# Kernel optimization log

Hardware: AMD Instinct MI355X
Metric: run time of the kernel (lower is better)

Reference implementation:

```python
import jax, jax.numpy as jnp
import numpy as np

NODES, NFEAT = 128, 256


def setup_inputs() -> dict:
    key = jax.random.key(0)
    k1, k2, k3, k4, k5, k6 = jax.random.split(key, 6)
    B = 512
    x = jax.random.normal(k1, (B, NODES, NFEAT), dtype=jnp.float32)
    adj = jax.random.uniform(k2, (B, NODES, NODES), dtype=jnp.float32)
    # GraphConvolution(nfeat, nfeat): weight [nfeat, nfeat], bias [nfeat]
    s = 1.0 / np.sqrt(NFEAT)
    gcn_w = jax.random.uniform(k3, (NFEAT, NFEAT), minval=-s, maxval=s, dtype=jnp.float32)
    gcn_b = jax.random.uniform(k4, (NFEAT,), minval=-s, maxval=s, dtype=jnp.float32)
    # fc: Linear(nfeat*nodes, nfeat), torch layout [out, in]
    s2 = 1.0 / np.sqrt(NFEAT * NODES)
    fc_w = jax.random.uniform(k5, (NFEAT, NFEAT * NODES), minval=-s2, maxval=s2, dtype=jnp.float32)
    fc_b = jax.random.uniform(k6, (NFEAT,), minval=-s2, maxval=s2, dtype=jnp.float32)
    return {"x": x, "adj": adj, "gcn_w": gcn_w, "gcn_b": gcn_b, "fc_w": fc_w, "fc_b": fc_b}


def reference(x, adj, gcn_w, gcn_b, fc_w, fc_b):
    B = x.shape[0]
    # Per-sample loop GCN fused as batched matmuls:
    # support = X @ W ; out = A @ support + b
    support = jnp.einsum('bnf,fg->bng', x, gcn_w)          # [B, nodes, nfeat]
    mid = jnp.einsum('bnm,bmg->bng', adj, support) + gcn_b  # [B, nodes, nfeat]
    # cat along dim0 then reshape(-1, nfeat*nodes) == per-graph flatten
    flat = mid.reshape(B, NODES * NFEAT)
    output = flat @ fc_w.T + fc_b                           # [B, nfeat]
    useful_input = x[:, 0, :]                               # [B, nfeat]
    return (output, useful_input, output)
```

## Files before the change

### kernel.cpp

```cpp
#include <hip/hip_runtime.h>

#define NODES 128
#define NFEAT 256
#define BATCH 512
#define KTOT  (NODES * NFEAT)
#define SPLIT 32
#define KCH   (KTOT / SPLIT)

typedef __bf16 bf16_t;
typedef bf16_t bf16x8 __attribute__((ext_vector_type(8)));
typedef float  f32x4  __attribute__((ext_vector_type(4)));

#define BK   32
#define LDK  40
#define LDM  136
#define TILE 128

__device__ __forceinline__ bf16x8 cvt8(const float4 a, const float4 b) {
    bf16x8 t;
    t[0] = (bf16_t)a.x; t[1] = (bf16_t)a.y; t[2] = (bf16_t)a.z; t[3] = (bf16_t)a.w;
    t[4] = (bf16_t)b.x; t[5] = (bf16_t)b.y; t[6] = (bf16_t)b.z; t[7] = (bf16_t)b.w;
    return t;
}

__device__ __forceinline__ void stage_f32(const float* __restrict__ src, int srcld,
                                          int k0, bf16_t* __restrict__ dst, int tid) {
#pragma unroll
    for (int i = 0; i < 2; i++) {
        int f = tid + i * 256;
        int r = f >> 2, c = f & 3;
        const float4 v0 = *(const float4*)(src + (size_t)r * srcld + k0 + c * 8);
        const float4 v1 = *(const float4*)(src + (size_t)r * srcld + k0 + c * 8 + 4);
        *(bf16x8*)(dst + r * LDK + c * 8) = cvt8(v0, v1);
    }
}

__device__ __forceinline__ void mfma_step(const bf16_t* As, const bf16_t* Bs,
                                          f32x4 acc[4][4], int lane) {
    const int l15 = lane & 15, q = lane >> 4;
    bf16x8 a[4], b[4];
#pragma unroll
    for (int i = 0; i < 4; i++)
        a[i] = *(const bf16x8*)(As + (i * 16 + l15) * LDK + q * 8);
#pragma unroll
    for (int j = 0; j < 4; j++)
        b[j] = *(const bf16x8*)(Bs + (j * 16 + l15) * LDK + q * 8);
#pragma unroll
    for (int i = 0; i < 4; i++)
#pragma unroll
        for (int j = 0; j < 4; j++)
            acc[i][j] = __builtin_amdgcn_mfma_f32_16x16x32_bf16(a[i], b[j], acc[i][j], 0, 0, 0);
}

__global__ __launch_bounds__(256)
void k_wt(const float* __restrict__ w, bf16_t* __restrict__ wT) {
    const int g0 = blockIdx.x * 4;
    const int k  = threadIdx.x;
    const float4 v = *(const float4*)(w + (size_t)k * NFEAT + g0);
    wT[(size_t)(g0 + 0) * NFEAT + k] = (bf16_t)v.x;
    wT[(size_t)(g0 + 1) * NFEAT + k] = (bf16_t)v.y;
    wT[(size_t)(g0 + 2) * NFEAT + k] = (bf16_t)v.z;
    wT[(size_t)(g0 + 3) * NFEAT + k] = (bf16_t)v.w;
}

__global__ __launch_bounds__(256, 2)
void k_fused12(const float* __restrict__ x, const float* __restrict__ adj,
               const bf16_t* __restrict__ wT, const float* __restrict__ gcn_b,
               bf16_t* __restrict__ mid) {
    __shared__ __align__(16) bf16_t As[TILE * LDK];
    __shared__ __align__(16) bf16_t Bs[TILE * LDK];
    __shared__ __align__(16) bf16_t Sb[TILE * LDM];
    const int n0  = blockIdx.x * TILE;
    const int b   = blockIdx.y;
    const int tid = threadIdx.x;
    const int lane = tid & 63, w = tid >> 6, wm = w & 1, wn = w >> 1;
    const int l15 = lane & 15, q = lane >> 4;
    const float* xb   = x   + (size_t)b * NODES * NFEAT;
    const float* adjb = adj + (size_t)b * NODES * NODES;

    f32x4 acc[4][4] = {};
    for (int k0 = 0; k0 < NFEAT; k0 += BK) {
        stage_f32(xb, NFEAT, k0, As, tid);
#pragma unroll
        for (int i = 0; i < 2; i++) {
            int f = tid + i * 256;
            int r = f >> 2, c = f & 3;
            *(bf16x8*)(Bs + r * LDK + c * 8) =
                *(const bf16x8*)(wT + (size_t)(n0 + r) * NFEAT + k0 + c * 8);
        }
        __syncthreads();
        mfma_step(As + wm * 64 * LDK, Bs + wn * 64 * LDK, acc, lane);
        __syncthreads();
    }
#pragma unroll
    for (int i = 0; i < 4; i++)
#pragma unroll
        for (int j = 0; j < 4; j++)
#pragma unroll
            for (int r = 0; r < 4; r++) {
                int m = wm * 64 + i * 16 + q * 4 + r;
                int g = wn * 64 + j * 16 + l15;
                Sb[g * LDM + m] = (bf16_t)acc[i][j][r];
            }
    __syncthreads();

    f32x4 acc2[4][4] = {};
    for (int k0 = 0; k0 < NODES; k0 += BK) {
        stage_f32(adjb, NODES, k0, As, tid);
        __syncthreads();
        bf16x8 a[4], bb[4];
#pragma unroll
        for (int i = 0; i < 4; i++)
            a[i] = *(const bf16x8*)(As + (wm * 64 + i * 16 + l15) * LDK + q * 8);
#pragma unroll
        for (int j = 0; j < 4; j++)
            bb[j] = *(const bf16x8*)(Sb + (wn * 64 + j * 16 + l15) * LDM + k0 + q * 8);
#pragma unroll
        for (int i = 0; i < 4; i++)
#pragma unroll
            for (int j = 0; j < 4; j++)
                acc2[i][j] = __builtin_amdgcn_mfma_f32_16x16x32_bf16(a[i], bb[j], acc2[i][j], 0, 0, 0);
        __syncthreads();
    }
    bf16_t* outb = mid + (size_t)b * NODES * NFEAT;
#pragma unroll
    for (int j = 0; j < 4; j++) {
        int g = n0 + wn * 64 + j * 16 + l15;
        float bias = gcn_b[g];
#pragma unroll
        for (int i = 0; i < 4; i++)
#pragma unroll
            for (int r = 0; r < 4; r++) {
                int node = wm * 64 + i * 16 + q * 4 + r;
                outb[(size_t)node * NFEAT + g] = (bf16_t)(acc2[i][j][r] + bias);
            }
    }
}

__global__ __launch_bounds__(256)
void k_out(const bf16_t* __restrict__ flat, const float* __restrict__ fcw,
           float* __restrict__ part) {
    __shared__ __align__(16) bf16_t As[TILE * LDK];
    __shared__ __align__(16) bf16_t Bs[TILE * LDK];
    const int m0 = blockIdx.x * TILE;
    const int n0 = blockIdx.y * TILE;
    const int s  = blockIdx.z;
    const int kb = s * KCH;
    const int tid = threadIdx.x;
    const int lane = tid & 63, w = tid >> 6, wm = w & 1, wn = w >> 1;
    f32x4 acc[4][4] = {};

    for (int k0 = kb; k0 < kb + KCH; k0 += BK) {
#pragma unroll
        for (int i = 0; i < 2; i++) {
            int f = tid + i * 256;
            int r = f >> 2, c = f & 3;
            *(bf16x8*)(As + r * LDK + c * 8) =
                *(const bf16x8*)(flat + (size_t)(m0 + r) * KTOT + k0 + c * 8);
        }
        stage_f32(fcw + (size_t)n0 * KTOT, KTOT, k0, Bs, tid);
        __syncthreads();
        mfma_step(As + wm * 64 * LDK, Bs + wn * 64 * LDK, acc, lane);
        __syncthreads();
    }
    const int l15 = lane & 15, q = lane >> 4;
    float* pb = part + (size_t)s * BATCH * NFEAT;
#pragma unroll
    for (int i = 0; i < 4; i++)
#pragma unroll
        for (int j = 0; j < 4; j++)
#pragma unroll
            for (int r = 0; r < 4; r++) {
                int bt = m0 + wm * 64 + i * 16 + q * 4 + r;
                int o  = n0 + wn * 64 + j * 16 + l15;
                pb[(size_t)bt * NFEAT + o] = acc[i][j][r];
            }
}

__global__ __launch_bounds__(256)
void k_reduce(const float* __restrict__ part, const float* __restrict__ fc_b,
              const float* __restrict__ x, float* __restrict__ out) {
    const int g = blockIdx.x * 256 + threadIdx.x;
    const int o = g & (NFEAT - 1), b = g >> 8;
    float s = fc_b[o];
#pragma unroll
    for (int i = 0; i < SPLIT; i++)
        s += part[(size_t)i * BATCH * NFEAT + g];
    out[g] = s;
    out[BATCH * NFEAT + g] = x[(size_t)b * NODES * NFEAT + o];
    out[2 * BATCH * NFEAT + g] = s;
}

extern "C" void kernel_launch(void* const* d_in, const int* in_sizes, int n_in,
                              void* d_out, int out_size, void* d_ws, size_t ws_size,
                              hipStream_t stream) {
    const float* x     = (const float*)d_in[0];
    const float* adj   = (const float*)d_in[1];
    const float* gcn_w = (const float*)d_in[2];
    const float* gcn_b = (const float*)d_in[3];
    const float* fc_w  = (const float*)d_in[4];
    const float* fc_b  = (const float*)d_in[5];
    float* out = (float*)d_out;

    bf16_t* wT   = (bf16_t*)d_ws;
    bf16_t* mid  = (bf16_t*)((char*)d_ws + 131072);
    float*  part = (float*)((char*)d_ws + 131072 + (size_t)BATCH * NODES * NFEAT * 2);

    k_wt     <<<dim3(64), dim3(256), 0, stream>>>(gcn_w, wT);
    k_fused12<<<dim3(2, BATCH), dim3(256), 0, stream>>>(x, adj, wT, gcn_b, mid);
    k_out    <<<dim3(4, 2, SPLIT), dim3(256), 0, stream>>>(mid, fc_w, part);
    k_reduce <<<dim3(BATCH), dim3(256), 0, stream>>>(part, fc_b, x, out);
}
```

Baseline: 221.2 us.

## Double-buffer GEMM staging with async global-to-LDS loads and swizzled fp32 tiles

Replaces register-staged fp32-to-bf16 conversion with direct global-to-LDS async loads of fp32 tiles, using an XOR-swizzled layout and converting to bf16 when fragments are read. Both the fused GCN kernel and the fc GEMM kernel now double-buffer LDS and prefetch the next K-slice, with one barrier per iteration instead of two. The gcn weight fragments and the flat activations are prefetched in registers. This aims to overlap memory latency with MFMA work, at the cost of more LDS (fp32 tiles), more registers, and conversion work repeated on every fragment read.

```diff
diff --git a/kernel.cpp b/kernel.cpp
--- a/kernel.cpp
+++ b/kernel.cpp
@@ -23,33 +23,28 @@
     return t;
 }
 
-__device__ __forceinline__ void stage_f32(const float* __restrict__ src, int srcld,
-                                          int k0, bf16_t* __restrict__ dst, int tid) {
-#pragma unroll
-    for (int i = 0; i < 2; i++) {
+__device__ __forceinline__ void gload16(const float* g, float* l) {
+    __builtin_amdgcn_global_load_lds(
+        (const __attribute__((address_space(1))) void*)g,
+        (__attribute__((address_space(3))) void*)l, 16, 0, 0);
+}
+
+__device__ __forceinline__ void stage_async(const float* __restrict__ src, int srcld,
+                                            int k0, float* __restrict__ lds, int tid) {
+#pragma unroll
+    for (int i = 0; i < 4; i++) {
         int f = tid + i * 256;
-        int r = f >> 2, c = f & 3;
-        const float4 v0 = *(const float4*)(src + (size_t)r * srcld + k0 + c * 8);
-        const float4 v1 = *(const float4*)(src + (size_t)r * srcld + k0 + c * 8 + 4);
-        *(bf16x8*)(dst + r * LDK + c * 8) = cvt8(v0, v1);
-    }
-}
-
-__device__ __forceinline__ void mfma_step(const bf16_t* As, const bf16_t* Bs,
-                                          f32x4 acc[4][4], int lane) {
-    const int l15 = lane & 15, q = lane >> 4;
-    bf16x8 a[4], b[4];
-#pragma unroll
-    for (int i = 0; i < 4; i++)
-        a[i] = *(const bf16x8*)(As + (i * 16 + l15) * LDK + q * 8);
-#pragma unroll
-    for (int j = 0; j < 4; j++)
-        b[j] = *(const bf16x8*)(Bs + (j * 16 + l15) * LDK + q * 8);
-#pragma unroll
-    for (int i = 0; i < 4; i++)
-#pragma unroll
-        for (int j = 0; j < 4; j++)
-            acc[i][j] = __builtin_amdgcn_mfma_f32_16x16x32_bf16(a[i], b[j], acc[i][j], 0, 0, 0);
+        int r = f >> 3, c = f & 7;
+        const float* g = src + (size_t)r * srcld + k0 + ((c ^ (r & 7)) << 2);
+        gload16(g, lds + ((f & ~63) << 2));
+    }
+}
+
+__device__ __forceinline__ bf16x8 frag_f32(const float* __restrict__ lds, int R, int q) {
+    const int s = R & 7;
+    const float4 u0 = *(const float4*)(lds + R * 32 + (((2 * q)     ^ s) << 2));
+    const float4 u1 = *(const float4*)(lds + R * 32 + (((2 * q + 1) ^ s) << 2));
+    return cvt8(u0, u1);
 }
 
 __global__ __launch_bounds__(256)
@@ -67,8 +62,7 @@
 void k_fused12(const float* __restrict__ x, const float* __restrict__ adj,
                const bf16_t* __restrict__ wT, const float* __restrict__ gcn_b,
                bf16_t* __restrict__ mid) {
-    __shared__ __align__(16) bf16_t As[TILE * LDK];
-    __shared__ __align__(16) bf16_t Bs[TILE * LDK];
+    __shared__ __align__(16) float  Axf[2][TILE * 32];
     __shared__ __align__(16) bf16_t Sb[TILE * LDM];
     const int n0  = blockIdx.x * TILE;
     const int b   = blockIdx.y;
@@ -78,20 +72,40 @@
     const float* xb   = x   + (size_t)b * NODES * NFEAT;
     const float* adjb = adj + (size_t)b * NODES * NODES;
 
+    const bf16_t* wrow[4];
+#pragma unroll
+    for (int j = 0; j < 4; j++)
+        wrow[j] = wT + (size_t)(n0 + wn * 64 + j * 16 + l15) * NFEAT + q * 8;
+
     f32x4 acc[4][4] = {};
+    stage_async(xb, NFEAT, 0, Axf[0], tid);
+    bf16x8 bcur[4], bnxt[4];
+#pragma unroll
+    for (int j = 0; j < 4; j++) bcur[j] = *(const bf16x8*)(wrow[j]);
+    __syncthreads();
+    int p = 0;
     for (int k0 = 0; k0 < NFEAT; k0 += BK) {
-        stage_f32(xb, NFEAT, k0, As, tid);
-#pragma unroll
-        for (int i = 0; i < 2; i++) {
-            int f = tid + i * 256;
-            int r = f >> 2, c = f & 3;
-            *(bf16x8*)(Bs + r * LDK + c * 8) =
-                *(const bf16x8*)(wT + (size_t)(n0 + r) * NFEAT + k0 + c * 8);
-        }
+        const int kn = k0 + BK;
+        const float* cur = Axf[p];
+        float* nxt = Axf[p ^ 1];
+        if (kn < NFEAT) stage_async(xb, NFEAT, kn, nxt, tid);
+        const int knc = (kn < NFEAT) ? kn : 0;
+#pragma unroll
+        for (int j = 0; j < 4; j++) bnxt[j] = *(const bf16x8*)(wrow[j] + knc);
+        bf16x8 a[4];
+#pragma unroll
+        for (int i = 0; i < 4; i++) a[i] = frag_f32(cur, wm * 64 + i * 16 + l15, q);
+#pragma unroll
+        for (int i = 0; i < 4; i++)
+#pragma unroll
+            for (int j = 0; j < 4; j++)
+                acc[i][j] = __builtin_amdgcn_mfma_f32_16x16x32_bf16(a[i], bcur[j], acc[i][j], 0, 0, 0);
         __syncthreads();
-        mfma_step(As + wm * 64 * LDK, Bs + wn * 64 * LDK, acc, lane);
-        __syncthreads();
-    }
+#pragma unroll
+        for (int j = 0; j < 4; j++) bcur[j] = bnxt[j];
+        p ^= 1;
+    }
+
 #pragma unroll
     for (int i = 0; i < 4; i++)
 #pragma unroll
@@ -102,16 +116,18 @@
                 int g = wn * 64 + j * 16 + l15;
                 Sb[g * LDM + m] = (bf16_t)acc[i][j][r];
             }
+    stage_async(adjb, NODES, 0, Axf[0], tid);
     __syncthreads();
-
     f32x4 acc2[4][4] = {};
+    p = 0;
     for (int k0 = 0; k0 < NODES; k0 += BK) {
-        stage_f32(adjb, NODES, k0, As, tid);
-        __syncthreads();
+        const int kn = k0 + BK;
+        const float* cur = Axf[p];
+        float* nxt = Axf[p ^ 1];
+        if (kn < NODES) stage_async(adjb, NODES, kn, nxt, tid);
         bf16x8 a[4], bb[4];
 #pragma unroll
-        for (int i = 0; i < 4; i++)
-            a[i] = *(const bf16x8*)(As + (wm * 64 + i * 16 + l15) * LDK + q * 8);
+        for (int i = 0; i < 4; i++) a[i] = frag_f32(cur, wm * 64 + i * 16 + l15, q);
 #pragma unroll
         for (int j = 0; j < 4; j++)
             bb[j] = *(const bf16x8*)(Sb + (wn * 64 + j * 16 + l15) * LDM + k0 + q * 8);
@@ -121,6 +137,7 @@
             for (int j = 0; j < 4; j++)
                 acc2[i][j] = __builtin_amdgcn_mfma_f32_16x16x32_bf16(a[i], bb[j], acc2[i][j], 0, 0, 0);
         __syncthreads();
+        p ^= 1;
     }
     bf16_t* outb = mid + (size_t)b * NODES * NFEAT;
 #pragma unroll
@@ -137,34 +154,54 @@
     }
 }
 
-__global__ __launch_bounds__(256)
+__global__ __launch_bounds__(256, 2)
 void k_out(const bf16_t* __restrict__ flat, const float* __restrict__ fcw,
            float* __restrict__ part) {
-    __shared__ __align__(16) bf16_t As[TILE * LDK];
-    __shared__ __align__(16) bf16_t Bs[TILE * LDK];
+    __shared__ __align__(16) bf16_t As2[2][TILE * LDK];
+    __shared__ __align__(16) float  Bsf[2][TILE * 32];
     const int m0 = blockIdx.x * TILE;
     const int n0 = blockIdx.y * TILE;
-    const int s  = blockIdx.z;
-    const int kb = s * KCH;
+    const int kb = blockIdx.z * KCH, kend = kb + KCH;
     const int tid = threadIdx.x;
     const int lane = tid & 63, w = tid >> 6, wm = w & 1, wn = w >> 1;
+    const int l15 = lane & 15, q = lane >> 4;
     f32x4 acc[4][4] = {};
-
-    for (int k0 = kb; k0 < kb + KCH; k0 += BK) {
-#pragma unroll
-        for (int i = 0; i < 2; i++) {
-            int f = tid + i * 256;
-            int r = f >> 2, c = f & 3;
-            *(bf16x8*)(As + r * LDK + c * 8) =
-                *(const bf16x8*)(flat + (size_t)(m0 + r) * KTOT + k0 + c * 8);
+    const float* fb = fcw + (size_t)n0 * KTOT;
+
+    const int ar = tid >> 2, ac = tid & 3;
+    bf16x8 a0 = *(const bf16x8*)(flat + (size_t)(m0 + ar) * KTOT + kb + ac * 8);
+    bf16x8 a1 = *(const bf16x8*)(flat + (size_t)(m0 + 64 + ar) * KTOT + kb + ac * 8);
+    stage_async(fb, KTOT, kb, Bsf[0], tid);
+    *(bf16x8*)(As2[0] + ar * LDK + ac * 8) = a0;
+    *(bf16x8*)(As2[0] + (64 + ar) * LDK + ac * 8) = a1;
+    __syncthreads();
+    int p = 0;
+    for (int k0 = kb; k0 < kend; k0 += BK) {
+        const int kn = k0 + BK;
+        const bool in = kn < kend;
+        const int knc = in ? kn : kb;
+        if (in) stage_async(fb, KTOT, kn, Bsf[p ^ 1], tid);
+        bf16x8 an0 = *(const bf16x8*)(flat + (size_t)(m0 + ar) * KTOT + knc + ac * 8);
+        bf16x8 an1 = *(const bf16x8*)(flat + (size_t)(m0 + 64 + ar) * KTOT + knc + ac * 8);
+        bf16x8 a[4], bbf[4];
+#pragma unroll
+        for (int i = 0; i < 4; i++)
+            a[i] = *(const bf16x8*)(As2[p] + (wm * 64 + i * 16 + l15) * LDK + q * 8);
+#pragma unroll
+        for (int j = 0; j < 4; j++) bbf[j] = frag_f32(Bsf[p], wn * 64 + j * 16 + l15, q);
+#pragma unroll
+        for (int i = 0; i < 4; i++)
+#pragma unroll
+            for (int j = 0; j < 4; j++)
+                acc[i][j] = __builtin_amdgcn_mfma_f32_16x16x32_bf16(a[i], bbf[j], acc[i][j], 0, 0, 0);
+        if (in) {
+            *(bf16x8*)(As2[p ^ 1] + ar * LDK + ac * 8) = an0;
+            *(bf16x8*)(As2[p ^ 1] + (64 + ar) * LDK + ac * 8) = an1;
         }
-        stage_f32(fcw + (size_t)n0 * KTOT, KTOT, k0, Bs, tid);
         __syncthreads();
-        mfma_step(As + wm * 64 * LDK, Bs + wn * 64 * LDK, acc, lane);
-        __syncthreads();
-    }
-    const int l15 = lane & 15, q = lane >> 4;
-    float* pb = part + (size_t)s * BATCH * NFEAT;
+        p ^= 1;
+    }
+    float* pb = part + (size_t)blockIdx.z * BATCH * NFEAT;
 #pragma unroll
     for (int i = 0; i < 4; i++)
 #pragma unroll
```

Result: no change. 224.1 us (+1.3%).

## Register-prefetch next tiles in GEMM loops, load W directly, bf16 split-K partials

Applied to the files above, without the earlier changes.

Adds register double-buffering to both stages of the fused GCN kernel and to the FC GEMM: each loop iteration issues the next tile's global loads before the MFMAs run on the current shared-memory tile. The GCN weight operand is now read straight from global into registers, which removes its shared-memory buffer and lets the occupancy hint rise to 3 blocks. The FC split-K factor doubles to 64 and partial sums are stored in bf16 to halve partial traffic. The costs are higher register pressure and lower precision in the split-K reduction.

```diff
diff --git a/kernel.cpp b/kernel.cpp
--- a/kernel.cpp
+++ b/kernel.cpp
@@ -4,7 +4,7 @@
 #define NFEAT 256
 #define BATCH 512
 #define KTOT  (NODES * NFEAT)
-#define SPLIT 32
+#define SPLIT 64
 #define KCH   (KTOT / SPLIT)
 
 typedef __bf16 bf16_t;
@@ -23,33 +23,39 @@
     return t;
 }
 
-__device__ __forceinline__ void stage_f32(const float* __restrict__ src, int srcld,
-                                          int k0, bf16_t* __restrict__ dst, int tid) {
-#pragma unroll
-    for (int i = 0; i < 2; i++) {
-        int f = tid + i * 256;
-        int r = f >> 2, c = f & 3;
-        const float4 v0 = *(const float4*)(src + (size_t)r * srcld + k0 + c * 8);
-        const float4 v1 = *(const float4*)(src + (size_t)r * srcld + k0 + c * 8 + 4);
-        *(bf16x8*)(dst + r * LDK + c * 8) = cvt8(v0, v1);
-    }
-}
-
-__device__ __forceinline__ void mfma_step(const bf16_t* As, const bf16_t* Bs,
-                                          f32x4 acc[4][4], int lane) {
-    const int l15 = lane & 15, q = lane >> 4;
-    bf16x8 a[4], b[4];
-#pragma unroll
-    for (int i = 0; i < 4; i++)
-        a[i] = *(const bf16x8*)(As + (i * 16 + l15) * LDK + q * 8);
-#pragma unroll
-    for (int j = 0; j < 4; j++)
-        b[j] = *(const bf16x8*)(Bs + (j * 16 + l15) * LDK + q * 8);
-#pragma unroll
-    for (int i = 0; i < 4; i++)
-#pragma unroll
-        for (int j = 0; j < 4; j++)
-            acc[i][j] = __builtin_amdgcn_mfma_f32_16x16x32_bf16(a[i], b[j], acc[i][j], 0, 0, 0);
+struct XT { float4 v[4]; };
+__device__ __forceinline__ void xload(const float* __restrict__ src, int ld, int k0,
+                                      int tid, XT& t) {
+#pragma unroll
+    for (int i = 0; i < 2; i++) {
+        int f = tid + i * 256, r = f >> 2, c = f & 3;
+        t.v[2 * i]     = *(const float4*)(src + (size_t)r * ld + k0 + c * 8);
+        t.v[2 * i + 1] = *(const float4*)(src + (size_t)r * ld + k0 + c * 8 + 4);
+    }
+}
+__device__ __forceinline__ void xstore(bf16_t* __restrict__ dst, int tid, const XT& t) {
+#pragma unroll
+    for (int i = 0; i < 2; i++) {
+        int f = tid + i * 256, r = f >> 2, c = f & 3;
+        *(bf16x8*)(dst + r * LDK + c * 8) = cvt8(t.v[2 * i], t.v[2 * i + 1]);
+    }
+}
+
+struct AT { bf16x8 v[2]; };
+__device__ __forceinline__ void aload(const bf16_t* __restrict__ src, int ld, int k0,
+                                      int tid, AT& t) {
+#pragma unroll
+    for (int i = 0; i < 2; i++) {
+        int f = tid + i * 256, r = f >> 2, c = f & 3;
+        t.v[i] = *(const bf16x8*)(src + (size_t)r * ld + k0 + c * 8);
+    }
+}
+__device__ __forceinline__ void astore(bf16_t* __restrict__ dst, int tid, const AT& t) {
+#pragma unroll
+    for (int i = 0; i < 2; i++) {
+        int f = tid + i * 256, r = f >> 2, c = f & 3;
+        *(bf16x8*)(dst + r * LDK + c * 8) = t.v[i];
+    }
 }
 
 __global__ __launch_bounds__(256)
@@ -63,12 +69,11 @@
     wT[(size_t)(g0 + 3) * NFEAT + k] = (bf16_t)v.w;
 }
 
-__global__ __launch_bounds__(256, 2)
+__global__ __launch_bounds__(256, 3)
 void k_fused12(const float* __restrict__ x, const float* __restrict__ adj,
                const bf16_t* __restrict__ wT, const float* __restrict__ gcn_b,
                bf16_t* __restrict__ mid) {
     __shared__ __align__(16) bf16_t As[TILE * LDK];
-    __shared__ __align__(16) bf16_t Bs[TILE * LDK];
     __shared__ __align__(16) bf16_t Sb[TILE * LDM];
     const int n0  = blockIdx.x * TILE;
     const int b   = blockIdx.y;
@@ -78,20 +83,45 @@
     const float* xb   = x   + (size_t)b * NODES * NFEAT;
     const float* adjb = adj + (size_t)b * NODES * NODES;
 
+    const bf16_t* wrow[4];
+#pragma unroll
+    for (int j = 0; j < 4; j++)
+        wrow[j] = wT + (size_t)(n0 + wn * 64 + j * 16 + l15) * NFEAT + q * 8;
+
     f32x4 acc[4][4] = {};
-    for (int k0 = 0; k0 < NFEAT; k0 += BK) {
-        stage_f32(xb, NFEAT, k0, As, tid);
-#pragma unroll
-        for (int i = 0; i < 2; i++) {
-            int f = tid + i * 256;
-            int r = f >> 2, c = f & 3;
-            *(bf16x8*)(Bs + r * LDK + c * 8) =
-                *(const bf16x8*)(wT + (size_t)(n0 + r) * NFEAT + k0 + c * 8);
+    {
+        XT xt; xload(xb, NFEAT, 0, tid, xt);
+        bf16x8 bcur[4], bnxt[4];
+#pragma unroll
+        for (int j = 0; j < 4; j++) bcur[j] = *(const bf16x8*)(wrow[j]);
+        xstore(As, tid, xt);
+        __syncthreads();
+        for (int k0 = 0; k0 < NFEAT; k0 += BK) {
+            const int kn = k0 + BK;
+            const bool in = kn < NFEAT;
+            XT xn;
+            if (in) xload(xb, NFEAT, kn, tid, xn);
+            const int knc = in ? kn : 0;
+#pragma unroll
+            for (int j = 0; j < 4; j++) bnxt[j] = *(const bf16x8*)(wrow[j] + knc);
+            bf16x8 a[4];
+#pragma unroll
+            for (int i = 0; i < 4; i++)
+                a[i] = *(const bf16x8*)(As + (wm * 64 + i * 16 + l15) * LDK + q * 8);
+#pragma unroll
+            for (int i = 0; i < 4; i++)
+#pragma unroll
+                for (int j = 0; j < 4; j++)
+                    acc[i][j] = __builtin_amdgcn_mfma_f32_16x16x32_bf16(a[i], bcur[j], acc[i][j], 0, 0, 0);
+            __syncthreads();
+            if (in) xstore(As, tid, xn);
+#pragma unroll
+            for (int j = 0; j < 4; j++) bcur[j] = bnxt[j];
+            __syncthreads();
         }
-        __syncthreads();
-        mfma_step(As + wm * 64 * LDK, Bs + wn * 64 * LDK, acc, lane);
-        __syncthreads();
-    }
+    }
+
+    XT at; xload(adjb, NODES, 0, tid, at);
 #pragma unroll
     for (int i = 0; i < 4; i++)
 #pragma unroll
@@ -103,11 +133,15 @@
                 Sb[g * LDM + m] = (bf16_t)acc[i][j][r];
             }
     __syncthreads();
+    xstore(As, tid, at);
+    __syncthreads();
 
     f32x4 acc2[4][4] = {};
     for (int k0 = 0; k0 < NODES; k0 += BK) {
-        stage_f32(adjb, NODES, k0, As, tid);
-        __syncthreads();
+        const int kn = k0 + BK;
+        const bool in = kn < NODES;
+        XT xn;
+        if (in) xload(adjb, NODES, kn, tid, xn);
         bf16x8 a[4], bb[4];
 #pragma unroll
         for (int i = 0; i < 4; i++)
@@ -120,6 +154,8 @@
 #pragma unroll
             for (int j = 0; j < 4; j++)
                 acc2[i][j] = __builtin_amdgcn_mfma_f32_16x16x32_bf16(a[i], bb[j], acc2[i][j], 0, 0, 0);
+        __syncthreads();
+        if (in) xstore(As, tid, xn);
         __syncthreads();
     }
     bf16_t* outb = mid + (size_t)b * NODES * NFEAT;
@@ -137,34 +173,48 @@
     }
 }
 
-__global__ __launch_bounds__(256)
+__global__ __launch_bounds__(256, 2)
 void k_out(const bf16_t* __restrict__ flat, const float* __restrict__ fcw,
-           float* __restrict__ part) {
+           bf16_t* __restrict__ part) {
     __shared__ __align__(16) bf16_t As[TILE * LDK];
     __shared__ __align__(16) bf16_t Bs[TILE * LDK];
     const int m0 = blockIdx.x * TILE;
     const int n0 = blockIdx.y * TILE;
-    const int s  = blockIdx.z;
-    const int kb = s * KCH;
+    const int kb = blockIdx.z * KCH, kend = kb + KCH;
     const int tid = threadIdx.x;
     const int lane = tid & 63, w = tid >> 6, wm = w & 1, wn = w >> 1;
+    const int l15 = lane & 15, q = lane >> 4;
     f32x4 acc[4][4] = {};
-
-    for (int k0 = kb; k0 < kb + KCH; k0 += BK) {
-#pragma unroll
-        for (int i = 0; i < 2; i++) {
-            int f = tid + i * 256;
-            int r = f >> 2, c = f & 3;
-            *(bf16x8*)(As + r * LDK + c * 8) =
-                *(const bf16x8*)(flat + (size_t)(m0 + r) * KTOT + k0 + c * 8);
-        }
-        stage_f32(fcw + (size_t)n0 * KTOT, KTOT, k0, Bs, tid);
-        __syncthreads();
-        mfma_step(As + wm * 64 * LDK, Bs + wn * 64 * LDK, acc, lane);
-        __syncthreads();
-    }
-    const int l15 = lane & 15, q = lane >> 4;
-    float* pb = part + (size_t)s * BATCH * NFEAT;
+    const bf16_t* fa = flat + (size_t)m0 * KTOT;
+    const float*  fb = fcw + (size_t)n0 * KTOT;
+
+    AT a0; aload(fa, KTOT, kb, tid, a0);
+    XT b0; xload(fb, KTOT, kb, tid, b0);
+    astore(As, tid, a0);
+    xstore(Bs, tid, b0);
+    __syncthreads();
+    for (int k0 = kb; k0 < kend; k0 += BK) {
+        const int kn = k0 + BK;
+        const bool in = kn < kend;
+        AT an; XT bn;
+        if (in) { aload(fa, KTOT, kn, tid, an); xload(fb, KTOT, kn, tid, bn); }
+        bf16x8 a[4], bbf[4];
+#pragma unroll
+        for (int i = 0; i < 4; i++)
+            a[i] = *(const bf16x8*)(As + (wm * 64 + i * 16 + l15) * LDK + q * 8);
+#pragma unroll
+        for (int j = 0; j < 4; j++)
+            bbf[j] = *(const bf16x8*)(Bs + (wn * 64 + j * 16 + l15) * LDK + q * 8);
+#pragma unroll
+        for (int i = 0; i < 4; i++)
+#pragma unroll
+            for (int j = 0; j < 4; j++)
+                acc[i][j] = __builtin_amdgcn_mfma_f32_16x16x32_bf16(a[i], bbf[j], acc[i][j], 0, 0, 0);
+        __syncthreads();
+        if (in) { astore(As, tid, an); xstore(Bs, tid, bn); }
+        __syncthreads();
+    }
+    bf16_t* pb = part + (size_t)blockIdx.z * BATCH * NFEAT;
 #pragma unroll
     for (int i = 0; i < 4; i++)
 #pragma unroll
@@ -173,19 +223,19 @@
             for (int r = 0; r < 4; r++) {
                 int bt = m0 + wm * 64 + i * 16 + q * 4 + r;
                 int o  = n0 + wn * 64 + j * 16 + l15;
-                pb[(size_t)bt * NFEAT + o] = acc[i][j][r];
+                pb[(size_t)bt * NFEAT + o] = (bf16_t)acc[i][j][r];
             }
 }
 
 __global__ __launch_bounds__(256)
-void k_reduce(const float* __restrict__ part, const float* __restrict__ fc_b,
+void k_reduce(const bf16_t* __restrict__ part, const float* __restrict__ fc_b,
               const float* __restrict__ x, float* __restrict__ out) {
     const int g = blockIdx.x * 256 + threadIdx.x;
     const int o = g & (NFEAT - 1), b = g >> 8;
     float s = fc_b[o];
 #pragma unroll
     for (int i = 0; i < SPLIT; i++)
-        s += part[(size_t)i * BATCH * NFEAT + g];
+        s += (float)part[(size_t)i * BATCH * NFEAT + g];
     out[g] = s;
     out[BATCH * NFEAT + g] = x[(size_t)b * NODES * NFEAT + o];
     out[2 * BATCH * NFEAT + g] = s;
@@ -204,7 +254,7 @@
 
     bf16_t* wT   = (bf16_t*)d_ws;
     bf16_t* mid  = (bf16_t*)((char*)d_ws + 131072);
-    float*  part = (float*)((char*)d_ws + 131072 + (size_t)BATCH * NODES * NFEAT * 2);
+    bf16_t* part = (bf16_t*)((char*)d_ws + 131072 + (size_t)BATCH * NODES * NFEAT * 2);
 
     k_wt     <<<dim3(64), dim3(256), 0, stream>>>(gcn_w, wT);
     k_fused12<<<dim3(2, BATCH), dim3(256), 0, stream>>>(x, adj, wT, gcn_b, mid);
```

Result: faster. 209.7 us (-5.2%).
